# Kernel optimization log

Measured on AMD Instinct MI355X. Metric: run time of the kernel, lower is better.

## Reference

```python
import jax, jax.numpy as jnp
import numpy as np
from jax import lax

B, L, H = 2, 1024, 2048
E, N, TR, K = 4096, 16, 128, 4


def setup_inputs() -> dict:
    key = jax.random.key(0)
    ks = jax.random.split(key, 10)
    s = lambda d: 1.0 / np.sqrt(d)
    return {
        "input_states": jax.random.normal(ks[0], (B, L, H), jnp.float32),
        "W_in": jax.random.normal(ks[1], (H, 2 * E), jnp.float32) * s(H),
        "conv_kernel": jax.random.normal(ks[2], (E, 1, K), jnp.float32) * s(K),
        "conv_bias": jax.random.normal(ks[3], (E,), jnp.float32) * 0.01,
        "W_x": jax.random.normal(ks[4], (E, TR + 2 * N), jnp.float32) * s(E),
        "W_dt": jax.random.normal(ks[5], (TR, E), jnp.float32) * s(TR),
        "b_dt": jax.random.normal(ks[6], (E,), jnp.float32) * 0.01,
        "W_out": jax.random.normal(ks[7], (E, H), jnp.float32) * s(E),
        "A_log": jax.random.uniform(ks[8], (E, N), jnp.float32, 0.0, 2.0),
        "D": jax.random.normal(ks[9], (E,), jnp.float32),
    }


def reference(input_states, W_in, conv_kernel, conv_bias, W_x, W_dt, b_dt,
              W_out, A_log, D):
    b, l, _ = input_states.shape
    dtype = input_states.dtype
    # in projection -> (b, 2E, l), split into hidden and gate streams
    proj = jnp.einsum("blh,he->bel", input_states, W_in)
    hidden, gate = jnp.split(proj, 2, axis=1)  # each (b, E, l)
    # depthwise causal conv1d (pad K-1, trim to l) + SiLU
    x = lax.conv_general_dilated(hidden, conv_kernel, window_strides=(1,),
                                 padding=((K - 1, K - 1),),
                                 feature_group_count=E)[..., :l]
    hidden = jax.nn.silu(x + conv_bias[None, :, None])  # (b, E, l)
    hs_ble = hidden.transpose(0, 2, 1)  # (b, l, E)
    # SSM parameters: dt (b,l,TR), Bm (b,l,N), Cm (b,l,N)
    ssm_p = jnp.einsum("ble,ed->bld", hs_ble, W_x)
    dt, Bm, Cm = jnp.split(ssm_p, [TR, TR + N], axis=-1)
    dts = jax.nn.softplus(jnp.einsum("blr,re->ble", dt, W_dt) + b_dt)  # (b,l,E)
    A = -jnp.exp(A_log.astype(jnp.float32))  # (E, N)
    # discretization
    dA = jnp.exp(dts[..., None] * A[None, None])            # (b, l, E, N)
    dBu = dts[..., None] * Bm[:, :, None, :] * hs_ble[..., None]  # (b, l, E, N)
    # selective scan over time (time-major for lax.scan)
    def step(state, inp):
        a, bu, c = inp  # (b,E,N), (b,E,N), (b,N)
        state = a * state + bu
        y = jnp.einsum("ben,bn->be", state.astype(dtype), c)
        return state, y
    init = jnp.zeros((b, E, N), dtype=dtype)
    _, ys = lax.scan(step, init, (dA.transpose(1, 0, 2, 3),
                                  dBu.transpose(1, 0, 2, 3),
                                  Cm.transpose(1, 0, 2)))  # ys: (l, b, E)
    scan_out = ys.transpose(1, 2, 0)  # (b, E, l)
    y = (scan_out + hidden * D[None, :, None]) * jax.nn.silu(gate)
    return jnp.einsum("bel,eh->blh", y, W_out)
```

## Files before the change

kernel.cpp:

```cpp
#include <hip/hip_runtime.h>
#include <cstddef>
#include <cstdint>

constexpr int B_  = 2;
constexpr int L_  = 1024;
constexpr int H_  = 2048;
constexpr int E_  = 4096;
constexpr int N_  = 16;
constexpr int TR_ = 128;
constexpr int M_  = B_ * L_;
constexpr int P2E = 2 * E_;
constexpr int SLD = TR_ + 2 * N_;
constexpr int CH_ = 32;
constexpr int CL_ = L_ / CH_;

typedef unsigned short u16;
using short8 = __attribute__((ext_vector_type(8))) short;
using f32x4  = __attribute__((ext_vector_type(4))) float;

__device__ __forceinline__ float siluf(float x) { return x / (1.f + expf(-x)); }
__device__ __forceinline__ float silu_fast(float x) { return x / (1.f + __expf(-x)); }
__device__ __forceinline__ float softplusf(float x) {
  return fmaxf(x, 0.f) + log1pf(expf(-fabsf(x)));
}
__device__ __forceinline__ u16 f2bf(float x) {
  union { float f; uint32_t u; } v; v.f = x;
  uint32_t r = v.u + 0x7FFFu + ((v.u >> 16) & 1u);
  return (u16)(r >> 16);
}
__device__ __forceinline__ float bf2f(u16 h) {
  union { uint32_t u; float f; } v; v.u = ((uint32_t)h) << 16; return v.f;
}
__device__ __forceinline__ void gll16(const u16* g, u16* l) {
  __builtin_amdgcn_global_load_lds(
      (const __attribute__((address_space(1))) void*)(const void*)g,
      (__attribute__((address_space(3))) void*)(void*)l, 16, 0, 0);
}

template<int BM, int BN, int BK, int TM, int TN, int EPI>
__global__ __launch_bounds__(256) void sgemm_k(
    const float* __restrict__ A, const float* __restrict__ B,
    float* __restrict__ C, int lda, int ldb, int ldc,
    const float* __restrict__ bias, int kchunk)
{
  __shared__ float As[BK][BM + 4];
  __shared__ float Bs[BK][BN];
  const int tid = threadIdx.x;
  const int tx  = tid & 15;
  const int ty  = tid >> 4;
  const int m0  = blockIdx.y * BM;
  const int n0  = blockIdx.x * BN;
  const int k00 = blockIdx.z * kchunk;

  float acc[TM][TN];
#pragma unroll
  for (int i = 0; i < TM; ++i)
#pragma unroll
    for (int j = 0; j < TN; ++j) acc[i][j] = 0.f;

  for (int k0 = k00; k0 < k00 + kchunk; k0 += BK) {
    constexpr int A4 = BM * BK / 4;
#pragma unroll
    for (int it = 0; it < (A4 + 255) / 256; ++it) {
      int i = it * 256 + tid;
      if ((A4 % 256 == 0) || (i < A4)) {
        int row = i / (BK / 4);
        int kc  = (i % (BK / 4)) * 4;
        float4 v = *reinterpret_cast<const float4*>(
            A + (size_t)(m0 + row) * lda + k0 + kc);
        As[kc + 0][row] = v.x; As[kc + 1][row] = v.y;
        As[kc + 2][row] = v.z; As[kc + 3][row] = v.w;
      }
    }
    constexpr int B4 = BK * BN / 4;
#pragma unroll
    for (int it = 0; it < (B4 + 255) / 256; ++it) {
      int i = it * 256 + tid;
      if ((B4 % 256 == 0) || (i < B4)) {
        int kr = i / (BN / 4);
        int nc = (i % (BN / 4)) * 4;
        *reinterpret_cast<float4*>(&Bs[kr][nc]) =
            *reinterpret_cast<const float4*>(
                B + (size_t)(k0 + kr) * ldb + n0 + nc);
      }
    }
    __syncthreads();
#pragma unroll
    for (int k = 0; k < BK; ++k) {
      float a[TM], bb[TN];
      const float* ap = &As[k][ty * TM];
      if constexpr (TM == 8) {
        float4 a0 = *reinterpret_cast<const float4*>(ap);
        float4 a1 = *reinterpret_cast<const float4*>(ap + 4);
        a[0]=a0.x; a[1]=a0.y; a[2]=a0.z; a[3]=a0.w;
        a[4]=a1.x; a[5]=a1.y; a[6]=a1.z; a[7]=a1.w;
      } else {
        float4 a0 = *reinterpret_cast<const float4*>(ap);
        a[0]=a0.x; a[1]=a0.y; a[2]=a0.z; a[3]=a0.w;
      }
      const float* bp = &Bs[k][tx * TN];
      if constexpr (TN == 4) {
        float4 b0 = *reinterpret_cast<const float4*>(bp);
        bb[0]=b0.x; bb[1]=b0.y; bb[2]=b0.z; bb[3]=b0.w;
      } else {
        float2 b0 = *reinterpret_cast<const float2*>(bp);
        bb[0]=b0.x; bb[1]=b0.y;
      }
#pragma unroll
      for (int i = 0; i < TM; ++i)
#pragma unroll
        for (int j = 0; j < TN; ++j) acc[i][j] = fmaf(a[i], bb[j], acc[i][j]);
    }
    __syncthreads();
  }

#pragma unroll
  for (int i = 0; i < TM; ++i) {
    int row = m0 + ty * TM + i;
    float* crow = C + (size_t)row * ldc + n0 + tx * TN;
    if constexpr (EPI == 2) {
#pragma unroll
      for (int j = 0; j < TN; ++j) atomicAdd(&crow[j], acc[i][j]);
    } else if constexpr (EPI == 1) {
      const float* brow = bias + n0 + tx * TN;
      float4 v;
      v.x = softplusf(acc[i][0] + brow[0]);
      v.y = softplusf(acc[i][1] + brow[1]);
      v.z = softplusf(acc[i][2] + brow[2]);
      v.w = softplusf(acc[i][3] + brow[3]);
      *reinterpret_cast<float4*>(crow) = v;
    } else {
      if constexpr (TN == 4) {
        float4 v; v.x=acc[i][0]; v.y=acc[i][1]; v.z=acc[i][2]; v.w=acc[i][3];
        *reinterpret_cast<float4*>(crow) = v;
      } else {
#pragma unroll
        for (int j = 0; j < TN; ++j) crow[j] = acc[i][j];
      }
    }
  }
}

__global__ __launch_bounds__(256) void decomp_k(
    const float* __restrict__ in, u16* __restrict__ hi, u16* __restrict__ lo,
    int n4)
{
  int i = blockIdx.x * 256 + threadIdx.x;
  if (i >= n4) return;
  float4 v = *reinterpret_cast<const float4*>(in + (size_t)i * 4);
  u16 h[4], l[4];
  float x[4] = {v.x, v.y, v.z, v.w};
#pragma unroll
  for (int j = 0; j < 4; ++j) {
    h[j] = f2bf(x[j]);
    l[j] = f2bf(x[j] - bf2f(h[j]));
  }
  uint32_t h0 = h[0] | ((uint32_t)h[1] << 16), h1 = h[2] | ((uint32_t)h[3] << 16);
  uint32_t l0 = l[0] | ((uint32_t)l[1] << 16), l1 = l[2] | ((uint32_t)l[3] << 16);
  *reinterpret_cast<uint2*>(hi + (size_t)i * 4) = make_uint2(h0, h1);
  *reinterpret_cast<uint2*>(lo + (size_t)i * 4) = make_uint2(l0, l1);
}

__global__ __launch_bounds__(256) void wdecomp_t_k(
    const float* __restrict__ W, u16* __restrict__ Whi, u16* __restrict__ Wlo,
    int KD, int ND)
{
  __shared__ float T[64][69];
  const int t  = threadIdx.x;
  const int n0 = blockIdx.x * 64;
  const int k0 = blockIdx.y * 64;
#pragma unroll
  for (int it = 0; it < 4; ++it) {
    int f  = it * 256 + t;
    int kk = f >> 4;
    int c  = (f & 15) * 4;
    float4 v = *reinterpret_cast<const float4*>(
        W + (size_t)(k0 + kk) * ND + n0 + c);
    T[kk][c] = v.x; T[kk][c+1] = v.y; T[kk][c+2] = v.z; T[kk][c+3] = v.w;
  }
  __syncthreads();
  const int nn   = t >> 2;
  const int kseg = (t & 3) * 16;
  const size_t off = (size_t)(n0 + nn) * KD + k0 + kseg;
#pragma unroll
  for (int half = 0; half < 2; ++half) {
    uint32_t hp[4], lp[4];
#pragma unroll
    for (int jj = 0; jj < 4; ++jj) {
      float x0 = T[kseg + half * 8 + jj * 2 + 0][nn];
      float x1 = T[kseg + half * 8 + jj * 2 + 1][nn];
      u16 h0 = f2bf(x0), h1 = f2bf(x1);
      u16 l0 = f2bf(x0 - bf2f(h0)), l1 = f2bf(x1 - bf2f(h1));
      hp[jj] = h0 | ((uint32_t)h1 << 16);
      lp[jj] = l0 | ((uint32_t)l1 << 16);
    }
    *reinterpret_cast<uint4*>(Whi + off + half * 8) =
        make_uint4(hp[0], hp[1], hp[2], hp[3]);
    *reinterpret_cast<uint4*>(Wlo + off + half * 8) =
        make_uint4(lp[0], lp[1], lp[2], lp[3]);
  }
}

__global__ __launch_bounds__(256) void gemm3bf_k(
    const u16* __restrict__ Ah, const u16* __restrict__ Al,
    const u16* __restrict__ Bh, const u16* __restrict__ Bl,
    float* __restrict__ C, int K, int ldc)
{
  __shared__ __align__(16) u16 sAh[128 * 32];
  __shared__ __align__(16) u16 sAl[128 * 32];
  __shared__ __align__(16) u16 sBh[128 * 32];
  __shared__ __align__(16) u16 sBl[128 * 32];

  const int tid  = threadIdx.x;
  const int lane = tid & 63;
  const int wid  = tid >> 6;
  const int wr   = wid >> 1, wc = wid & 1;

  const int nwg = gridDim.x;
  const int q8  = nwg >> 3;
  const int wg  = (blockIdx.x & 7) * q8 + (blockIdx.x >> 3);
  const int tm  = wg & 15;
  const int tn  = wg >> 4;
  const int m0  = tm * 128;
  const int n0  = tn * 128;

  const int dr = lane >> 2;
  const int sw = (lane & 3) ^ ((lane >> 3) & 3);
  const int r1 = wid * 16 + dr;
  const int r2 = r1 + 64;

  const u16* ga1 = Ah + (size_t)(m0 + r1) * K + sw * 8;
  const u16* ga2 = Ah + (size_t)(m0 + r2) * K + sw * 8;
  const u16* gl1 = Al + (size_t)(m0 + r1) * K + sw * 8;
  const u16* gl2 = Al + (size_t)(m0 + r2) * K + sw * 8;
  const u16* gb1 = Bh + (size_t)(n0 + r1) * K + sw * 8;
  const u16* gb2 = Bh + (size_t)(n0 + r2) * K + sw * 8;
  const u16* gc1 = Bl + (size_t)(n0 + r1) * K + sw * 8;
  const u16* gc2 = Bl + (size_t)(n0 + r2) * K + sw * 8;

  u16* dA1 = sAh + (wid * 16) * 32;
  u16* dA2 = sAh + (64 + wid * 16) * 32;
  u16* dL1 = sAl + (wid * 16) * 32;
  u16* dL2 = sAl + (64 + wid * 16) * 32;
  u16* dB1 = sBh + (wid * 16) * 32;
  u16* dB2 = sBh + (64 + wid * 16) * 32;
  u16* dC1 = sBl + (wid * 16) * 32;
  u16* dC2 = sBl + (64 + wid * 16) * 32;

  const int fr = lane & 15;
  const int ph = (lane >> 4) ^ ((fr >> 1) & 3);
  const int offA = (wr * 64 + fr) * 32 + ph * 8;
  const int offB = (wc * 64 + fr) * 32 + ph * 8;

  f32x4 acc[4][4] = {};

  for (int k0 = 0; k0 < K; k0 += 32) {
    __syncthreads();
    gll16(ga1 + k0, dA1);  gll16(ga2 + k0, dA2);
    gll16(gl1 + k0, dL1);  gll16(gl2 + k0, dL2);
    gll16(gb1 + k0, dB1);  gll16(gb2 + k0, dB2);
    gll16(gc1 + k0, dC1);  gll16(gc2 + k0, dC2);
    __syncthreads();

    short8 bhf[4], blf[4];
#pragma unroll
    for (int nc = 0; nc < 4; ++nc) {
      bhf[nc] = *reinterpret_cast<const short8*>(&sBh[offB + nc * 512]);
      blf[nc] = *reinterpret_cast<const short8*>(&sBl[offB + nc * 512]);
    }
#pragma unroll
    for (int mr = 0; mr < 4; ++mr) {
      short8 ahf = *reinterpret_cast<const short8*>(&sAh[offA + mr * 512]);
      short8 alf = *reinterpret_cast<const short8*>(&sAl[offA + mr * 512]);
#pragma unroll
      for (int nc = 0; nc < 4; ++nc) {
        acc[mr][nc] = __builtin_amdgcn_mfma_f32_16x16x32_bf16(ahf, bhf[nc], acc[mr][nc], 0, 0, 0);
        acc[mr][nc] = __builtin_amdgcn_mfma_f32_16x16x32_bf16(ahf, blf[nc], acc[mr][nc], 0, 0, 0);
        acc[mr][nc] = __builtin_amdgcn_mfma_f32_16x16x32_bf16(alf, bhf[nc], acc[mr][nc], 0, 0, 0);
      }
    }
  }

#pragma unroll
  for (int mr = 0; mr < 4; ++mr) {
    const int rowb = m0 + wr * 64 + mr * 16 + ((lane >> 4) << 2);
#pragma unroll
    for (int nc = 0; nc < 4; ++nc) {
      const int col = n0 + wc * 64 + nc * 16 + fr;
      float* cp = C + (size_t)rowb * ldc + col;
#pragma unroll
      for (int i = 0; i < 4; ++i) cp[(size_t)i * ldc] = acc[mr][nc][i];
    }
  }
}

__global__ __launch_bounds__(256) void conv_silu_k(
    const float* __restrict__ proj, const float* __restrict__ ck,
    const float* __restrict__ cb, float* __restrict__ hc)
{
  const int idx = blockIdx.x * 256 + threadIdx.x;
  const int e = idx & (E_ - 1);
  const int m = idx >> 12;
  const int l = m & (L_ - 1);
  const float c0 = ck[e * 4 + 0], c1 = ck[e * 4 + 1];
  const float c2 = ck[e * 4 + 2], c3 = ck[e * 4 + 3];
  const float* pcol = proj + (size_t)m * P2E + e;
  float acc = cb[e];
  if (l >= 3) acc = fmaf(pcol[-3 * P2E], c0, acc);
  if (l >= 2) acc = fmaf(pcol[-2 * P2E], c1, acc);
  if (l >= 1) acc = fmaf(pcol[-1 * P2E], c2, acc);
  acc = fmaf(pcol[0], c3, acc);
  hc[(size_t)m * E_ + e] = siluf(acc);
}

__global__ __launch_bounds__(256) void scan_p1_k(
    const float* __restrict__ hc, const float* __restrict__ ssm,
    const float* __restrict__ A_log, const float* __restrict__ dts,
    float* __restrict__ Pbuf, float* __restrict__ Qbuf)
{
  __shared__ float sB[CL_][16];
  const int tid = threadIdx.x;
  const int bid = blockIdx.x;
  const int e   = ((bid & 15) << 8) + tid;
  const int c   = (bid >> 4) & (CH_ - 1);
  const int b   = bid >> 9;
  const int m0  = b * L_ + c * CL_;

  if (tid < CL_ * 4) {
    int s = tid >> 2, q = tid & 3;
    *reinterpret_cast<float4*>(&sB[s][q * 4]) =
        *reinterpret_cast<const float4*>(
            &ssm[(size_t)(m0 + s) * SLD + TR_ + q * 4]);
  }
  __syncthreads();

  float Aen[N_];
#pragma unroll
  for (int q = 0; q < 4; ++q) {
    float4 av = *reinterpret_cast<const float4*>(&A_log[e * N_ + q * 4]);
    Aen[q*4+0] = -expf(av.x); Aen[q*4+1] = -expf(av.y);
    Aen[q*4+2] = -expf(av.z); Aen[q*4+3] = -expf(av.w);
  }

  float P[N_], Q[N_];
#pragma unroll
  for (int n = 0; n < N_; ++n) { P[n] = 1.f; Q[n] = 0.f; }

  float dt_c = dts[(size_t)m0 * E_ + e];
  float h_c  = hc [(size_t)m0 * E_ + e];
  for (int s = 0; s < CL_; ++s) {
    const int sn = (s + 1 < CL_) ? s + 1 : s;
    const float dt_n = dts[(size_t)(m0 + sn) * E_ + e];
    const float h_n  = hc [(size_t)(m0 + sn) * E_ + e];
    const float dth = dt_c * h_c;
#pragma unroll
    for (int q = 0; q < 4; ++q) {
      const float4 bv = *reinterpret_cast<const float4*>(&sB[s][q * 4]);
      const float bx[4] = {bv.x, bv.y, bv.z, bv.w};
#pragma unroll
      for (int j = 0; j < 4; ++j) {
        const int n = q * 4 + j;
        const float a = __expf(dt_c * Aen[n]);
        Q[n] = fmaf(a, Q[n], dth * bx[j]);
        P[n] *= a;
      }
    }
    dt_c = dt_n; h_c = h_n;
  }

  const size_t ob = (((size_t)b * CH_ + c) * N_) * E_ + e;
#pragma unroll
  for (int n = 0; n < N_; ++n) {
    Pbuf[ob + (size_t)n * E_] = P[n];
    Qbuf[ob + (size_t)n * E_] = Q[n];
  }
}

__global__ __launch_bounds__(256) void scan_p3_k(
    const float* __restrict__ hc, const float* __restrict__ ssm,
    const float* __restrict__ proj, const float* __restrict__ A_log,
    const float* __restrict__ Dvec, const float* __restrict__ dts,
    const float* __restrict__ Pbuf, const float* __restrict__ Qbuf,
    u16* __restrict__ yhi, u16* __restrict__ ylo)
{
  __shared__ float sBC[CL_][32];
  const int tid = threadIdx.x;
  const int bid = blockIdx.x;
  const int e   = ((bid & 15) << 8) + tid;
  const int c   = (bid >> 4) & (CH_ - 1);
  const int b   = bid >> 9;
  const int m0  = b * L_ + c * CL_;

  {
    int s = tid >> 3, q = tid & 7;
    *reinterpret_cast<float4*>(&sBC[s][q * 4]) =
        *reinterpret_cast<const float4*>(
            &ssm[(size_t)(m0 + s) * SLD + TR_ + q * 4]);
  }
  __syncthreads();

  float Aen[N_];
#pragma unroll
  for (int q = 0; q < 4; ++q) {
    float4 av = *reinterpret_cast<const float4*>(&A_log[e * N_ + q * 4]);
    Aen[q*4+0] = -expf(av.x); Aen[q*4+1] = -expf(av.y);
    Aen[q*4+2] = -expf(av.z); Aen[q*4+3] = -expf(av.w);
  }
  const float De = Dvec[e];

  float st[N_];
#pragma unroll
  for (int n = 0; n < N_; ++n) st[n] = 0.f;
  for (int cc = 0; cc < c; ++cc) {
    const size_t ob = (((size_t)b * CH_ + cc) * N_) * E_ + e;
#pragma unroll
    for (int n = 0; n < N_; ++n)
      st[n] = fmaf(Pbuf[ob + (size_t)n * E_], st[n], Qbuf[ob + (size_t)n * E_]);
  }

  float dt_c = dts[(size_t)m0 * E_ + e];
  float h_c  = hc [(size_t)m0 * E_ + e];
  float g_c  = proj[(size_t)m0 * P2E + E_ + e];
  for (int s = 0; s < CL_; ++s) {
    const int sn = (s + 1 < CL_) ? s + 1 : s;
    const float dt_n = dts[(size_t)(m0 + sn) * E_ + e];
    const float h_n  = hc [(size_t)(m0 + sn) * E_ + e];
    const float g_n  = proj[(size_t)(m0 + sn) * P2E + E_ + e];
    const float dth = dt_c * h_c;
    float y = h_c * De;
#pragma unroll
    for (int q = 0; q < 4; ++q) {
      const float4 bv = *reinterpret_cast<const float4*>(&sBC[s][q * 4]);
      const float4 cv = *reinterpret_cast<const float4*>(&sBC[s][16 + q * 4]);
      const float bx[4] = {bv.x, bv.y, bv.z, bv.w};
      const float cx[4] = {cv.x, cv.y, cv.z, cv.w};
#pragma unroll
      for (int j = 0; j < 4; ++j) {
        const int n = q * 4 + j;
        const float a = __expf(dt_c * Aen[n]);
        st[n] = fmaf(a, st[n], dth * bx[j]);
        y = fmaf(st[n], cx[j], y);
      }
    }
    const float res = y * silu_fast(g_c);
    const u16 hv = f2bf(res);
    const size_t yo = (size_t)(m0 + s) * E_ + e;
    yhi[yo] = hv;
    ylo[yo] = f2bf(res - bf2f(hv));
    dt_c = dt_n; h_c = h_n; g_c = g_n;
  }
}

__global__ __launch_bounds__(256) void scan_serial_k(
    const float* __restrict__ hc, const float* __restrict__ ssm,
    const float* __restrict__ proj, const float* __restrict__ A_log,
    const float* __restrict__ Dvec, const float* __restrict__ dts,
    float* __restrict__ yf)
{
  const int tid = threadIdx.x;
  const int n  = tid & 15;
  const int ge = blockIdx.x * 16 + (tid >> 4);
  const int b  = ge >> 12;
  const int e  = ge & (E_ - 1);
  const float Aen = -expf(A_log[e * N_ + n]);
  const float De  = Dvec[e];
  float state = 0.f;
  const int mbase = b * L_;
  for (int l = 0; l < L_; ++l) {
    const int m = mbase + l;
    const float dt = dts[(size_t)m * E_ + e];
    const float h  = hc[(size_t)m * E_ + e];
    const float Bm = ssm[(size_t)m * SLD + TR_ + n];
    const float Cm = ssm[(size_t)m * SLD + TR_ + N_ + n];
    state = fmaf(expf(dt * Aen), state, dt * Bm * h);
    float yp = state * Cm;
    yp += __shfl_xor(yp, 1);
    yp += __shfl_xor(yp, 2);
    yp += __shfl_xor(yp, 4);
    yp += __shfl_xor(yp, 8);
    const float g   = proj[(size_t)m * P2E + E_ + e];
    const float res = (yp + h * De) * siluf(g);
    if (n == 0) yf[(size_t)m * E_ + e] = res;
  }
}

extern "C" void kernel_launch(void* const* d_in, const int* in_sizes, int n_in,
                              void* d_out, int out_size, void* d_ws, size_t ws_size,
                              hipStream_t stream)
{
  const float* x_in  = (const float*)d_in[0];
  const float* W_in  = (const float*)d_in[1];
  const float* ck    = (const float*)d_in[2];
  const float* cb    = (const float*)d_in[3];
  const float* W_x   = (const float*)d_in[4];
  const float* W_dt  = (const float*)d_in[5];
  const float* b_dt  = (const float*)d_in[6];
  const float* W_out = (const float*)d_in[7];
  const float* A_log = (const float*)d_in[8];
  const float* Dvec  = (const float*)d_in[9];
  float* out = (float*)d_out;
  float* ws  = (float*)d_ws;

  float* proj = ws;
  float* hc   = proj + (size_t)M_ * P2E;
  float* dts  = hc   + (size_t)M_ * E_;
  float* ssm  = dts  + (size_t)M_ * E_;

  u16* regA  = (u16*)(ssm + (size_t)M_ * SLD);
  u16* x_hi  = regA;
  u16* x_lo  = regA + (size_t)M_ * H_;
  u16* Wo_hi = regA;
  u16* Wo_lo = regA + (size_t)H_ * E_;
  u16* regB  = regA + 16777216;
  u16* Wi_hi = regB;
  u16* Wi_lo = regB + (size_t)P2E * H_;
  u16* y_hi  = regB;
  u16* y_lo  = regB + (size_t)M_ * E_;
  float* Pbuf = (float*)(regB + 16777216);
  float* Qbuf = Pbuf + (size_t)B_ * CH_ * E_ * N_;

  const size_t need_bf =
      ((size_t)M_ * P2E + 2 * (size_t)M_ * E_ + (size_t)M_ * SLD) * 4 +
      (16777216ULL + 33554432ULL) * 2;

  hipMemsetAsync(ssm, 0, (size_t)M_ * SLD * sizeof(float), stream);

  if (ws_size >= need_bf) {
    decomp_k<<<(M_ * H_ / 4 + 255) / 256, 256, 0, stream>>>(
        x_in, x_hi, x_lo, M_ * H_ / 4);
    wdecomp_t_k<<<dim3(P2E / 64, H_ / 64), 256, 0, stream>>>(
        W_in, Wi_hi, Wi_lo, H_, P2E);
    gemm3bf_k<<<(M_ / 128) * (P2E / 128), 256, 0, stream>>>(
        x_hi, x_lo, Wi_hi, Wi_lo, proj, H_, P2E);
    conv_silu_k<<<(M_ * E_) / 256, 256, 0, stream>>>(proj, ck, cb, hc);
    sgemm_k<64,32,16,4,2,2><<<dim3(SLD/32, M_/64, 8), 256, 0, stream>>>(
        hc, W_x, ssm, E_, SLD, SLD, nullptr, E_/8);
    sgemm_k<128,64,16,8,4,1><<<dim3(E_/64, M_/128, 1), 256, 0, stream>>>(
        ssm, W_dt, dts, SLD, E_, E_, b_dt, TR_);
    wdecomp_t_k<<<dim3(H_ / 64, E_ / 64), 256, 0, stream>>>(
        W_out, Wo_hi, Wo_lo, E_, H_);
    scan_p1_k<<<B_ * CH_ * (E_ / 256), 256, 0, stream>>>(
        hc, ssm, A_log, dts, Pbuf, Qbuf);
    scan_p3_k<<<B_ * CH_ * (E_ / 256), 256, 0, stream>>>(
        hc, ssm, proj, A_log, Dvec, dts, Pbuf, Qbuf, y_hi, y_lo);
    gemm3bf_k<<<(M_ / 128) * (H_ / 128), 256, 0, stream>>>(
        y_hi, y_lo, Wo_hi, Wo_lo, out, E_, H_);
  } else {
    size_t base_f = (size_t)M_ * P2E + 2 * (size_t)M_ * E_ + (size_t)M_ * SLD;
    size_t need   = (base_f + (size_t)M_ * E_) * sizeof(float);
    float* yb = (ws_size >= need) ? (ssm + (size_t)M_ * SLD) : dts;
    sgemm_k<128,64,16,8,4,0><<<dim3(P2E/64, M_/128, 1), 256, 0, stream>>>(
        x_in, W_in, proj, H_, P2E, P2E, nullptr, H_);
    conv_silu_k<<<(M_ * E_) / 256, 256, 0, stream>>>(proj, ck, cb, hc);
    sgemm_k<64,32,16,4,2,2><<<dim3(SLD/32, M_/64, 8), 256, 0, stream>>>(
        hc, W_x, ssm, E_, SLD, SLD, nullptr, E_/8);
    sgemm_k<128,64,16,8,4,1><<<dim3(E_/64, M_/128, 1), 256, 0, stream>>>(
        ssm, W_dt, dts, SLD, E_, E_, b_dt, TR_);
    scan_serial_k<<<(B_ * E_) / 16, 256, 0, stream>>>(
        hc, ssm, proj, A_log, Dvec, dts, yb);
    sgemm_k<128,64,16,8,4,0><<<dim3(H_/64, M_/128, 1), 256, 0, stream>>>(
        yb, W_out, out, E_, H_, H_, nullptr, E_);
  }
}
```

Before: 832.7 us.

## Move x_proj and dt_proj GEMMs to split-bf16 MFMA with split-K reduce

Replaces the two FP32 SIMT GEMMs (hidden·W_x and dt·W_dt) with 3-term bf16 hi/lo MFMA GEMMs. The conv kernel now also emits bf16 hi/lo copies of the hidden states. The x_proj GEMM uses a 16-way split-K with a separate reduction kernel that also decomposes dt, instead of atomics plus a memset. The dt GEMM fuses bias and softplus into its epilogue. This trades extra decomposition traffic, the partial-sum buffer and additional kernel launches for matrix-core throughput on GEMMs that were previously scalar.

```diff
diff --git a/kernel.cpp b/kernel.cpp
--- a/kernel.cpp
+++ b/kernel.cpp
@@ -13,6 +13,7 @@
 constexpr int SLD = TR_ + 2 * N_;
 constexpr int CH_ = 32;
 constexpr int CL_ = L_ / CH_;
+constexpr int XKZ = 16;
 
 typedef unsigned short u16;
 using short8 = __attribute__((ext_vector_type(8))) short;
@@ -161,6 +162,7 @@
   *reinterpret_cast<uint2*>(lo + (size_t)i * 4) = make_uint2(l0, l1);
 }
 
+template<bool GUARD>
 __global__ __launch_bounds__(256) void wdecomp_t_k(
     const float* __restrict__ W, u16* __restrict__ Whi, u16* __restrict__ Wlo,
     int KD, int ND)
@@ -174,13 +176,18 @@
     int f  = it * 256 + t;
     int kk = f >> 4;
     int c  = (f & 15) * 4;
-    float4 v = *reinterpret_cast<const float4*>(
-        W + (size_t)(k0 + kk) * ND + n0 + c);
-    T[kk][c] = v.x; T[kk][c+1] = v.y; T[kk][c+2] = v.z; T[kk][c+3] = v.w;
+    if (!GUARD || (n0 + c < ND)) {
+      float4 v = *reinterpret_cast<const float4*>(
+          W + (size_t)(k0 + kk) * ND + n0 + c);
+      T[kk][c] = v.x; T[kk][c+1] = v.y; T[kk][c+2] = v.z; T[kk][c+3] = v.w;
+    } else {
+      T[kk][c] = 0.f; T[kk][c+1] = 0.f; T[kk][c+2] = 0.f; T[kk][c+3] = 0.f;
+    }
   }
   __syncthreads();
   const int nn   = t >> 2;
   const int kseg = (t & 3) * 16;
+  if (GUARD && (n0 + nn >= ND)) return;
   const size_t off = (size_t)(n0 + nn) * KD + k0 + kseg;
 #pragma unroll
   for (int half = 0; half < 2; ++half) {
@@ -201,10 +208,11 @@
   }
 }
 
+template<int EPI>
 __global__ __launch_bounds__(256) void gemm3bf_k(
     const u16* __restrict__ Ah, const u16* __restrict__ Al,
     const u16* __restrict__ Bh, const u16* __restrict__ Bl,
-    float* __restrict__ C, int K, int ldc)
+    float* __restrict__ C, int K, int ldc, const float* __restrict__ bias)
 {
   __shared__ __align__(16) u16 sAh[128 * 32];
   __shared__ __align__(16) u16 sAl[128 * 32];
@@ -288,15 +296,124 @@
     for (int nc = 0; nc < 4; ++nc) {
       const int col = n0 + wc * 64 + nc * 16 + fr;
       float* cp = C + (size_t)rowb * ldc + col;
-#pragma unroll
-      for (int i = 0; i < 4; ++i) cp[(size_t)i * ldc] = acc[mr][nc][i];
-    }
+      if constexpr (EPI == 1) {
+        const float bv = bias[col];
+#pragma unroll
+        for (int i = 0; i < 4; ++i)
+          cp[(size_t)i * ldc] = softplusf(acc[mr][nc][i] + bv);
+      } else {
+#pragma unroll
+        for (int i = 0; i < 4; ++i) cp[(size_t)i * ldc] = acc[mr][nc][i];
+      }
+    }
+  }
+}
+
+__global__ __launch_bounds__(256) void gemmx_k(
+    const u16* __restrict__ Ah, const u16* __restrict__ Al,
+    const u16* __restrict__ Bh, const u16* __restrict__ Bl,
+    float* __restrict__ part)
+{
+  constexpr int LDK = 40;
+  __shared__ __align__(16) u16 sAh[128 * LDK];
+  __shared__ __align__(16) u16 sAl[128 * LDK];
+  __shared__ __align__(16) u16 sBh[160 * LDK];
+  __shared__ __align__(16) u16 sBl[160 * LDK];
+
+  const int tid  = threadIdx.x;
+  const int lane = tid & 63;
+  const int wid  = tid >> 6;
+  const int mt   = blockIdx.x & 15;
+  const int kz   = blockIdx.x >> 4;
+  const int m0   = mt * 128;
+  const int k00  = kz * (E_ / XKZ);
+  const int fr   = lane & 15;
+  const int fk   = (lane >> 4) * 8;
+
+  f32x4 acc[2][10] = {};
+
+  for (int k0 = k00; k0 < k00 + E_ / XKZ; k0 += 32) {
+    __syncthreads();
+#pragma unroll
+    for (int it = 0; it < 2; ++it) {
+      int i = it * 256 + tid;
+      int row = i >> 2, c = (i & 3) * 8;
+      size_t go = (size_t)(m0 + row) * E_ + k0 + c;
+      *reinterpret_cast<uint4*>(&sAh[row * LDK + c]) =
+          *reinterpret_cast<const uint4*>(Ah + go);
+      *reinterpret_cast<uint4*>(&sAl[row * LDK + c]) =
+          *reinterpret_cast<const uint4*>(Al + go);
+    }
+#pragma unroll
+    for (int it = 0; it < 3; ++it) {
+      int i = it * 256 + tid;
+      if (i < 640) {
+        int row = i >> 2, c = (i & 3) * 8;
+        size_t go = (size_t)row * E_ + k0 + c;
+        *reinterpret_cast<uint4*>(&sBh[row * LDK + c]) =
+            *reinterpret_cast<const uint4*>(Bh + go);
+        *reinterpret_cast<uint4*>(&sBl[row * LDK + c]) =
+            *reinterpret_cast<const uint4*>(Bl + go);
+      }
+    }
+    __syncthreads();
+
+    short8 a_h[2], a_l[2];
+#pragma unroll
+    for (int mr = 0; mr < 2; ++mr) {
+      int row = wid * 32 + mr * 16 + fr;
+      a_h[mr] = *reinterpret_cast<const short8*>(&sAh[row * LDK + fk]);
+      a_l[mr] = *reinterpret_cast<const short8*>(&sAl[row * LDK + fk]);
+    }
+#pragma unroll
+    for (int nc = 0; nc < 10; ++nc) {
+      int row = nc * 16 + fr;
+      short8 b_h = *reinterpret_cast<const short8*>(&sBh[row * LDK + fk]);
+      short8 b_l = *reinterpret_cast<const short8*>(&sBl[row * LDK + fk]);
+#pragma unroll
+      for (int mr = 0; mr < 2; ++mr) {
+        acc[mr][nc] = __builtin_amdgcn_mfma_f32_16x16x32_bf16(a_h[mr], b_h, acc[mr][nc], 0, 0, 0);
+        acc[mr][nc] = __builtin_amdgcn_mfma_f32_16x16x32_bf16(a_h[mr], b_l, acc[mr][nc], 0, 0, 0);
+        acc[mr][nc] = __builtin_amdgcn_mfma_f32_16x16x32_bf16(a_l[mr], b_h, acc[mr][nc], 0, 0, 0);
+      }
+    }
+  }
+
+#pragma unroll
+  for (int mr = 0; mr < 2; ++mr) {
+    const int rowb = m0 + wid * 32 + mr * 16 + ((lane >> 4) << 2);
+#pragma unroll
+    for (int nc = 0; nc < 10; ++nc) {
+      const int col = nc * 16 + fr;
+      float* pp = part + ((size_t)kz * M_ + rowb) * SLD + col;
+#pragma unroll
+      for (int i = 0; i < 4; ++i) pp[(size_t)i * SLD] = acc[mr][nc][i];
+    }
+  }
+}
+
+__global__ __launch_bounds__(256) void xreduce_k(
+    const float* __restrict__ part, float* __restrict__ ssm,
+    u16* __restrict__ sdt_hi, u16* __restrict__ sdt_lo)
+{
+  const int t = blockIdx.x * 256 + threadIdx.x;
+  float s = 0.f;
+#pragma unroll
+  for (int z = 0; z < XKZ; ++z) s += part[(size_t)z * M_ * SLD + t];
+  ssm[t] = s;
+  const int col = t % SLD;
+  if (col < TR_) {
+    const int m = t / SLD;
+    const u16 hv = f2bf(s);
+    sdt_hi[(size_t)m * TR_ + col] = hv;
+    sdt_lo[(size_t)m * TR_ + col] = f2bf(s - bf2f(hv));
   }
 }
 
 __global__ __launch_bounds__(256) void conv_silu_k(
     const float* __restrict__ proj, const float* __restrict__ ck,
-    const float* __restrict__ cb, float* __restrict__ hc)
+    const float* __restrict__ cb, float* __restrict__ hc,
+    u16* __restrict__ hchi, u16* __restrict__ hclo)
 {
   const int idx = blockIdx.x * 256 + threadIdx.x;
   const int e = idx & (E_ - 1);
@@ -310,7 +427,12 @@
   if (l >= 2) acc = fmaf(pcol[-2 * P2E], c1, acc);
   if (l >= 1) acc = fmaf(pcol[-1 * P2E], c2, acc);
   acc = fmaf(pcol[0], c3, acc);
-  hc[(size_t)m * E_ + e] = siluf(acc);
+  const float r = siluf(acc);
+  const size_t o = (size_t)m * E_ + e;
+  hc[o] = r;
+  const u16 hv = f2bf(r);
+  hchi[o] = hv;
+  hclo[o] = f2bf(r - bf2f(hv));
 }
 
 __global__ __launch_bounds__(256) void scan_p1_k(
@@ -514,44 +636,62 @@
   u16* regB  = regA + 16777216;
   u16* Wi_hi = regB;
   u16* Wi_lo = regB + (size_t)P2E * H_;
+  u16* hc_hi = regB;
+  u16* hc_lo = regB + (size_t)M_ * E_;
   u16* y_hi  = regB;
   u16* y_lo  = regB + (size_t)M_ * E_;
+  float* part = (float*)(regB + 16777216);
   float* Pbuf = (float*)(regB + 16777216);
   float* Qbuf = Pbuf + (size_t)B_ * CH_ * E_ * N_;
+  u16* su      = regB + 16777216 + 2 * (size_t)XKZ * M_ * SLD;
+  u16* Wxt_hi  = su;
+  u16* Wxt_lo  = su + 655360;
+  u16* Wdtt_hi = su + 1310720;
+  u16* Wdtt_lo = su + 1835008;
+  u16* sdt_hi  = su + 2359296;
+  u16* sdt_lo  = su + 2621440;
 
   const size_t need_bf =
       ((size_t)M_ * P2E + 2 * (size_t)M_ * E_ + (size_t)M_ * SLD) * 4 +
       (16777216ULL + 33554432ULL) * 2;
 
-  hipMemsetAsync(ssm, 0, (size_t)M_ * SLD * sizeof(float), stream);
-
   if (ws_size >= need_bf) {
     decomp_k<<<(M_ * H_ / 4 + 255) / 256, 256, 0, stream>>>(
         x_in, x_hi, x_lo, M_ * H_ / 4);
-    wdecomp_t_k<<<dim3(P2E / 64, H_ / 64), 256, 0, stream>>>(
+    wdecomp_t_k<false><<<dim3(P2E / 64, H_ / 64), 256, 0, stream>>>(
         W_in, Wi_hi, Wi_lo, H_, P2E);
-    gemm3bf_k<<<(M_ / 128) * (P2E / 128), 256, 0, stream>>>(
-        x_hi, x_lo, Wi_hi, Wi_lo, proj, H_, P2E);
-    conv_silu_k<<<(M_ * E_) / 256, 256, 0, stream>>>(proj, ck, cb, hc);
-    sgemm_k<64,32,16,4,2,2><<<dim3(SLD/32, M_/64, 8), 256, 0, stream>>>(
-        hc, W_x, ssm, E_, SLD, SLD, nullptr, E_/8);
-    sgemm_k<128,64,16,8,4,1><<<dim3(E_/64, M_/128, 1), 256, 0, stream>>>(
-        ssm, W_dt, dts, SLD, E_, E_, b_dt, TR_);
-    wdecomp_t_k<<<dim3(H_ / 64, E_ / 64), 256, 0, stream>>>(
+    gemm3bf_k<0><<<(M_ / 128) * (P2E / 128), 256, 0, stream>>>(
+        x_hi, x_lo, Wi_hi, Wi_lo, proj, H_, P2E, nullptr);
+    conv_silu_k<<<(M_ * E_) / 256, 256, 0, stream>>>(
+        proj, ck, cb, hc, hc_hi, hc_lo);
+    wdecomp_t_k<true><<<dim3(3, E_ / 64), 256, 0, stream>>>(
+        W_x, Wxt_hi, Wxt_lo, E_, SLD);
+    wdecomp_t_k<false><<<dim3(E_ / 64, TR_ / 64), 256, 0, stream>>>(
+        W_dt, Wdtt_hi, Wdtt_lo, TR_, E_);
+    gemmx_k<<<16 * XKZ, 256, 0, stream>>>(
+        hc_hi, hc_lo, Wxt_hi, Wxt_lo, part);
+    xreduce_k<<<(M_ * SLD) / 256, 256, 0, stream>>>(
+        part, ssm, sdt_hi, sdt_lo);
+    gemm3bf_k<1><<<(M_ / 128) * (E_ / 128), 256, 0, stream>>>(
+        sdt_hi, sdt_lo, Wdtt_hi, Wdtt_lo, dts, TR_, E_, b_dt);
+    wdecomp_t_k<false><<<dim3(H_ / 64, E_ / 64), 256, 0, stream>>>(
         W_out, Wo_hi, Wo_lo, E_, H_);
     scan_p1_k<<<B_ * CH_ * (E_ / 256), 256, 0, stream>>>(
         hc, ssm, A_log, dts, Pbuf, Qbuf);
     scan_p3_k<<<B_ * CH_ * (E_ / 256), 256, 0, stream>>>(
         hc, ssm, proj, A_log, Dvec, dts, Pbuf, Qbuf, y_hi, y_lo);
-    gemm3bf_k<<<(M_ / 128) * (H_ / 128), 256, 0, stream>>>(
-        y_hi, y_lo, Wo_hi, Wo_lo, out, E_, H_);
+    gemm3bf_k<0><<<(M_ / 128) * (H_ / 128), 256, 0, stream>>>(
+        y_hi, y_lo, Wo_hi, Wo_lo, out, E_, H_, nullptr);
   } else {
+    hipMemsetAsync(ssm, 0, (size_t)M_ * SLD * sizeof(float), stream);
     size_t base_f = (size_t)M_ * P2E + 2 * (size_t)M_ * E_ + (size_t)M_ * SLD;
     size_t need   = (base_f + (size_t)M_ * E_) * sizeof(float);
     float* yb = (ws_size >= need) ? (ssm + (size_t)M_ * SLD) : dts;
     sgemm_k<128,64,16,8,4,0><<<dim3(P2E/64, M_/128, 1), 256, 0, stream>>>(
         x_in, W_in, proj, H_, P2E, P2E, nullptr, H_);
-    conv_silu_k<<<(M_ * E_) / 256, 256, 0, stream>>>(proj, ck, cb, hc);
+    conv_silu_k<<<(M_ * E_) / 256, 256, 0, stream>>>(
+        proj, ck, cb, hc, (u16*)(ssm + (size_t)M_ * SLD),
+        (u16*)(ssm + (size_t)M_ * SLD) + (size_t)M_ * E_);
     sgemm_k<64,32,16,4,2,2><<<dim3(SLD/32, M_/64, 8), 256, 0, stream>>>(
         hc, W_x, ssm, E_, SLD, SLD, nullptr, E_/8);
     sgemm_k<128,64,16,8,4,1><<<dim3(E_/64, M_/128, 1), 256, 0, stream>>>(
```

Result: faster. 778.2 us (-6.5%).
